# Kernel optimization log

Hardware: AMD Instinct MI355X
Metric: run time of the kernel (lower is better)

## Reference

```python
import jax, jax.numpy as jnp
import numpy as np

E = 512        # emb_size
H = 2 * E      # LSTM units
B = 512        # beam/query batch (batched Python-loop states)
K = 32         # padded candidates per state
T = 8          # max_path_length
N_ENT = 50000
N_REL = 5000


def setup_inputs() -> dict:
    key = jax.random.key(0)
    ks = jax.random.split(key, 12)
    f32 = jnp.float32
    ent_emb = jax.random.normal(ks[0], (N_ENT, E), f32) * 0.05
    rel_emb = jax.random.normal(ks[1], (N_REL, E), f32) * 0.05
    relation = jax.random.normal(ks[2], (B, E), f32) * 0.05
    Wx = jax.random.normal(ks[3], (H, 4 * H), f32) * 0.02
    Wh = jax.random.normal(ks[4], (H, 4 * H), f32) * 0.02
    b = jnp.zeros((4 * H,), f32)
    W1 = jax.random.normal(ks[5], (4 * E, 3 * E), f32) * 0.02
    b1 = jnp.zeros((3 * E,), f32)
    W2 = jax.random.normal(ks[6], (3 * E, 2 * E), f32) * 0.02
    b2 = jnp.zeros((2 * E,), f32)
    current_ids = jax.random.randint(ks[7], (T, B), 0, N_ENT)
    prev_rel_ids = jax.random.randint(ks[8], (T, B), 0, N_REL)
    cand_rel_ids = jax.random.randint(ks[9], (T, B, K), 0, N_REL)
    cand_ent_ids = jax.random.randint(ks[10], (T, B, K), 0, N_ENT)
    return {
        "ent_emb": ent_emb, "rel_emb": rel_emb, "relation": relation,
        "Wx": Wx, "Wh": Wh, "b": b,
        "W1": W1, "b1": b1, "W2": W2, "b2": b2,
        "current_ids": current_ids, "prev_rel_ids": prev_rel_ids,
        "cand_rel_ids": cand_rel_ids, "cand_ent_ids": cand_ent_ids,
    }


def reference(ent_emb, rel_emb, relation, Wx, Wh, b, W1, b1, W2, b2,
              current_ids, prev_rel_ids, cand_rel_ids, cand_ent_ids):
    Bh = relation.shape[0]
    units = Wh.shape[0]
    h0 = jnp.zeros((Bh, units), ent_emb.dtype)
    c0 = jnp.zeros((Bh, units), ent_emb.dtype)

    def step(carry, xs):
        h, c = carry
        cur, prl, crel, cent = xs
        # LSTMCell input: concat(prev relation vec, current entity vec)  [B, 2E]
        x = jnp.concatenate([rel_emb[prl], ent_emb[cur]], axis=-1)
        z = x @ Wx + h @ Wh + b                      # [B, 4H], keras gate order i,f,g,o
        i_, f_, g_, o_ = jnp.split(z, 4, axis=-1)
        c = jax.nn.sigmoid(f_) * c + jax.nn.sigmoid(i_) * jnp.tanh(g_)
        h = jax.nn.sigmoid(o_) * jnp.tanh(c)
        # posterior MLP on concat(ent, history, relation)  [B, 4E] -> [B, 2E]
        feat = jax.nn.relu(jnp.concatenate([ent_emb[cur], h, relation], axis=-1) @ W1 + b1)
        feat = jax.nn.relu(feat @ W2 + b2)
        # candidate embeddings: concat(rel vec, to-entity vec)  [B, K, 2E]
        cand = jnp.concatenate([rel_emb[crel], ent_emb[cent]], axis=-1)
        probs = jax.nn.softmax(jnp.einsum('bkd,bd->bk', cand, feat), axis=-1)
        return (h, c), probs

    _, probs = jax.lax.scan(step, (h0, c0),
                            (current_ids, prev_rel_ids, cand_rel_ids, cand_ent_ids))
    return probs  # [T, B, K]
```

## Files before the change

kernel.cpp:

```cpp
#include <hip/hip_runtime.h>
#include <stdint.h>

typedef __attribute__((ext_vector_type(4))) float f32x4;
typedef __attribute__((ext_vector_type(8))) __bf16 bf16x8;
typedef __attribute__((ext_vector_type(8))) unsigned short u16x8;
typedef __attribute__((ext_vector_type(4))) unsigned short u16x4;

__device__ __forceinline__ float b2f(unsigned short u) {
  unsigned int x = ((unsigned int)u) << 16;
  float f; __builtin_memcpy(&f, &x, 4); return f;
}
__device__ __forceinline__ unsigned short f2b(float f) {
  unsigned int x; __builtin_memcpy(&x, &f, 4);
  x += 0x7fffu + ((x >> 16) & 1u);
  return (unsigned short)(x >> 16);
}
__device__ __forceinline__ float sigmoidf(float x) {
  return 1.f / (1.f + __expf(-x));
}
__device__ __forceinline__ float tanh_fast(float x) {
  return 1.f - 2.f / (1.f + __expf(2.f * x));
}

__global__ __launch_bounds__(256) void transpose_f2b(
    const float* __restrict__ in, unsigned short* __restrict__ out,
    int R, int C) {
  __shared__ unsigned short tile[64][72];
  const int r0 = blockIdx.y * 64, c0 = blockIdx.x * 64;
  const int tid = threadIdx.x;
  const int r = tid >> 3;
  const int c8 = (tid & 7) * 8;
#pragma unroll
  for (int i = 0; i < 2; i++) {
    const float* src = in + (size_t)(r0 + r + 32*i) * C + c0 + c8;
    f32x4 a = *(const f32x4*)src;
    f32x4 b = *(const f32x4*)(src + 4);
    unsigned short tmp[8];
#pragma unroll
    for (int j = 0; j < 4; j++) { tmp[j] = f2b(a[j]); tmp[4+j] = f2b(b[j]); }
    *(u16x8*)(&tile[r + 32*i][c8]) = *(u16x8*)tmp;
  }
  __syncthreads();
#pragma unroll
  for (int i = 0; i < 2; i++) {
    const int ro = r + 32*i;
    unsigned short tmp[8];
#pragma unroll
    for (int j = 0; j < 8; j++) tmp[j] = tile[c8 + j][ro];
    *(u16x8*)(out + (size_t)(c0 + ro) * R + r0 + c8) = *(u16x8*)tmp;
  }
}

__global__ void gather_all(const float* __restrict__ ent,
                           const float* __restrict__ rel,
                           const float* __restrict__ relation,
                           const int* __restrict__ cur, const int* __restrict__ prl,
                           unsigned short* __restrict__ Xall,
                           unsigned short* __restrict__ ERall) {
  const int row = blockIdx.x;
  const int b = row & 511;
  const int tid = threadIdx.x;
  const int ci = cur[row], ri = prl[row];
  const float* xsrc = (tid < 64) ? (rel + (size_t)ri * 512 + tid * 8)
                                 : (ent + (size_t)ci * 512 + (tid - 64) * 8);
  const float* esrc = (tid < 64) ? (ent + (size_t)ci * 512 + tid * 8)
                                 : (relation + (size_t)b * 512 + (tid - 64) * 8);
  f32x4 xa = *(const f32x4*)xsrc, xb = *(const f32x4*)(xsrc + 4);
  f32x4 ea = *(const f32x4*)esrc, eb = *(const f32x4*)(esrc + 4);
  unsigned short xt[8], et[8];
#pragma unroll
  for (int j = 0; j < 4; j++) {
    xt[j] = f2b(xa[j]); xt[4+j] = f2b(xb[j]);
    et[j] = f2b(ea[j]); et[4+j] = f2b(eb[j]);
  }
  *(u16x8*)(Xall + (size_t)row * 1024 + tid * 8) = *(u16x8*)xt;
  *(u16x8*)(ERall + (size_t)row * 1024 + tid * 8) = *(u16x8*)et;
}

template<bool HAS_PRE, bool HAS_BIAS, bool DO_RELU, bool PERM_B>
__global__ __launch_bounds__(256) void gemm_bf16(
    const unsigned short* __restrict__ A, int lda,
    const unsigned short* __restrict__ BT, int ldb,
    int K, int ksplit, int koff0, int koff1,
    const unsigned short* __restrict__ pre, int ldpre,
    const float* __restrict__ bias,
    unsigned short* __restrict__ Cout, int ldc) {
  __shared__ unsigned short As[128][72];
  __shared__ unsigned short Bs[128][72];
  const int tid = threadIdx.x;
  const int lane = tid & 63;
  const int w = tid >> 6;
  const int wr = w >> 1, wc = w & 1;
  const int m0 = blockIdx.y * 128, n0 = blockIdx.x * 128;
  f32x4 acc[4][4] = {};
  const int rs = tid >> 3;
  const int cs = (tid & 7) * 8;

  for (int k0 = 0; k0 < K; k0 += 64) {
    const int keff = (k0 < ksplit) ? (k0 + koff0) : (k0 + koff1);
#pragma unroll
    for (int i = 0; i < 4; i++)
      *(u16x8*)(&As[rs + 32*i][cs]) =
          *(const u16x8*)(A + (size_t)(m0 + rs + 32*i) * lda + k0 + cs);
#pragma unroll
    for (int i = 0; i < 4; i++) {
      const int brow = n0 + rs + 32*i;
      const int prow = PERM_B ? (((brow & 3) << 10) + (brow >> 2)) : brow;
      *(u16x8*)(&Bs[rs + 32*i][cs]) =
          *(const u16x8*)(BT + (size_t)prow * ldb + keff + cs);
    }
    __syncthreads();
#pragma unroll
    for (int ks = 0; ks < 2; ks++) {
      const int kb = ks * 32 + (lane >> 4) * 8;
      bf16x8 af[4], bfr[4];
#pragma unroll
      for (int m = 0; m < 4; m++)
        af[m] = *reinterpret_cast<const bf16x8*>(&As[wr*64 + m*16 + (lane & 15)][kb]);
#pragma unroll
      for (int n = 0; n < 4; n++)
        bfr[n] = *reinterpret_cast<const bf16x8*>(&Bs[wc*64 + n*16 + (lane & 15)][kb]);
#pragma unroll
      for (int m = 0; m < 4; m++)
#pragma unroll
        for (int n = 0; n < 4; n++)
          acc[m][n] = __builtin_amdgcn_mfma_f32_16x16x32_bf16(af[m], bfr[n], acc[m][n], 0, 0, 0);
    }
    __syncthreads();
  }

  const int cn = lane & 15, rb = (lane >> 4) * 4;
#pragma unroll
  for (int m = 0; m < 4; m++) {
#pragma unroll
    for (int n = 0; n < 4; n++) {
      const int gn = n0 + wc*64 + n*16 + cn;
#pragma unroll
      for (int r = 0; r < 4; r++) {
        const int gm = m0 + wr*64 + m*16 + rb + r;
        float v = acc[m][n][r];
        if (HAS_PRE)  v += b2f(pre[(size_t)gm * ldpre + gn]);
        if (HAS_BIAS) v += bias[gn];
        if (DO_RELU)  v = v > 0.f ? v : 0.f;
        Cout[(size_t)gm * ldc + gn] = f2b(v);
      }
    }
  }
}

__global__ __launch_bounds__(512) void zgemm_lstm(
    const unsigned short* __restrict__ A,
    const unsigned short* __restrict__ BT,
    const unsigned short* __restrict__ pre,
    const float* __restrict__ bias,
    unsigned short* __restrict__ Hout,
    float* __restrict__ Cst) {
  __shared__ unsigned short As[2][64][72];
  __shared__ unsigned short Bs[2][128][72];
  __shared__ f32x4 accL[8][256];
  const int tid = threadIdx.x;
  const int lane = tid & 63;
  const int w = tid >> 6;
  const int q = w >> 2;
  const int wq = w & 3;
  const int wr = wq >> 1, wc = wq & 1;
  const int m0 = blockIdx.y * 64, n0 = blockIdx.x * 128;
  f32x4 acc[2][4] = {};
  const int tq = tid & 255;
  const int rs = tq >> 3;
  const int cs = (tq & 7) * 8;

  for (int k0 = 0; k0 < 512; k0 += 64) {
    const int kk = q * 512 + k0;
#pragma unroll
    for (int i = 0; i < 2; i++)
      *(u16x8*)(&As[q][rs + 32*i][cs]) =
          *(const u16x8*)(A + (size_t)(m0 + rs + 32*i) * 1024 + kk + cs);
#pragma unroll
    for (int i = 0; i < 4; i++) {
      const int brow = n0 + rs + 32*i;
      const int prow = ((brow & 3) << 10) + (brow >> 2);
      *(u16x8*)(&Bs[q][rs + 32*i][cs]) =
          *(const u16x8*)(BT + (size_t)prow * 1024 + kk + cs);
    }
    __syncthreads();
#pragma unroll
    for (int ks = 0; ks < 2; ks++) {
      const int kb = ks * 32 + (lane >> 4) * 8;
      bf16x8 af[2], bfr[4];
#pragma unroll
      for (int m = 0; m < 2; m++)
        af[m] = *reinterpret_cast<const bf16x8*>(&As[q][wr*32 + m*16 + (lane & 15)][kb]);
#pragma unroll
      for (int n = 0; n < 4; n++)
        bfr[n] = *reinterpret_cast<const bf16x8*>(&Bs[q][wc*64 + n*16 + (lane & 15)][kb]);
#pragma unroll
      for (int m = 0; m < 2; m++)
#pragma unroll
        for (int n = 0; n < 4; n++)
          acc[m][n] = __builtin_amdgcn_mfma_f32_16x16x32_bf16(af[m], bfr[n], acc[m][n], 0, 0, 0);
    }
    __syncthreads();
  }

  if (q == 1) {
#pragma unroll
    for (int m = 0; m < 2; m++)
#pragma unroll
      for (int n = 0; n < 4; n++)
        accL[m*4 + n][tq] = acc[m][n];
  }
  __syncthreads();
  if (q == 0) {
    const int cn = lane & 15, rb = (lane >> 4) * 4, g = lane & 3;
#pragma unroll
    for (int m = 0; m < 2; m++) {
#pragma unroll
      for (int n = 0; n < 4; n++) {
        const f32x4 s4 = accL[m*4 + n][tq];
        const int gn = n0 + wc*64 + n*16 + cn;
        const int u = gn >> 2;
        const float gb = bias[g * 1024 + u];
        const int row0 = m0 + wr*32 + m*16 + rb;
        const float v0 = acc[m][n][0] + s4[0] + b2f(pre[(size_t)(row0+0) * 4096 + gn]) + gb;
        const float v1 = acc[m][n][1] + s4[1] + b2f(pre[(size_t)(row0+1) * 4096 + gn]) + gb;
        const float v2 = acc[m][n][2] + s4[2] + b2f(pre[(size_t)(row0+2) * 4096 + gn]) + gb;
        const float v3 = acc[m][n][3] + s4[3] + b2f(pre[(size_t)(row0+3) * 4096 + gn]) + gb;
        auto sel = [&](int idx) {
          return idx == 0 ? v0 : idx == 1 ? v1 : idx == 2 ? v2 : v3;
        };
        const float own = sel(g);
        const float r1 = __shfl_xor(sel(g ^ 1), 1);
        const float r2 = __shfl_xor(sel(g ^ 2), 2);
        const float r3 = __shfl_xor(sel(g ^ 3), 3);
        const float zi = g==0 ? own : g==1 ? r1 : g==2 ? r2 : r3;
        const float zf = g==0 ? r1  : g==1 ? own: g==2 ? r3 : r2;
        const float zg_= g==0 ? r2  : g==1 ? r3 : g==2 ? own: r1;
        const float zo = g==0 ? r3  : g==1 ? r2 : g==2 ? r1 : own;
        const size_t hidx = (size_t)(row0 + g) * 1024 + u;
        const float cnew = sigmoidf(zf) * Cst[hidx] + sigmoidf(zi) * tanh_fast(zg_);
        const float h = sigmoidf(zo) * tanh_fast(cnew);
        Cst[hidx] = cnew;
        Hout[hidx] = f2b(h);
      }
    }
  }
}

__global__ void lstm_gate0(const unsigned short* __restrict__ P1_,
                           const float* __restrict__ bias,
                           float* __restrict__ C, unsigned short* __restrict__ H) {
  const int idx = blockIdx.x * 256 + threadIdx.x;
  const int b = idx >> 10, u = idx & 1023;
  u16x4 z4 = *(const u16x4*)(P1_ + (size_t)b * 4096 + 4 * u);
  const float i_ = b2f(z4[0]) + bias[u];
  const float g_ = b2f(z4[2]) + bias[2048 + u];
  const float o_ = b2f(z4[3]) + bias[3072 + u];
  const float c = sigmoidf(i_) * tanh_fast(g_);
  const float h = sigmoidf(o_) * tanh_fast(c);
  C[idx] = c;
  H[idx] = f2b(h);
}

__global__ __launch_bounds__(256) void score_softmax(
    const unsigned short* __restrict__ F2,
    const float* __restrict__ rel,
    const float* __restrict__ ent,
    const int* __restrict__ crel, const int* __restrict__ cent,
    float* __restrict__ outp) {
  const int b = blockIdx.x;
  const int tid = threadIdx.x;
  const int lane = tid & 63, w = tid >> 6;
  __shared__ float feat[1024];
  __shared__ float logits[32];
  {
    u16x4 fv = ((const u16x4*)(F2 + (size_t)b * 1024))[tid];
#pragma unroll
    for (int j = 0; j < 4; j++) feat[tid * 4 + j] = b2f(fv[j]);
  }
  __syncthreads();
  for (int k = w; k < 32; k += 4) {
    const int ri = crel[b * 32 + k], ei = cent[b * 32 + k];
    const float* rp = rel + (size_t)ri * 512 + lane * 8;
    const float* ep = ent + (size_t)ei * 512 + lane * 8;
    f32x4 r0 = *(const f32x4*)rp, r1 = *(const f32x4*)(rp + 4);
    f32x4 e0 = *(const f32x4*)ep, e1 = *(const f32x4*)(ep + 4);
    float sum = 0.f;
#pragma unroll
    for (int j = 0; j < 4; j++) {
      sum += r0[j] * feat[lane * 8 + j];
      sum += r1[j] * feat[lane * 8 + 4 + j];
      sum += e0[j] * feat[512 + lane * 8 + j];
      sum += e1[j] * feat[512 + lane * 8 + 4 + j];
    }
#pragma unroll
    for (int off = 32; off; off >>= 1) sum += __shfl_down(sum, off, 64);
    if (lane == 0) logits[k] = sum;
  }
  __syncthreads();
  if (tid < 32) {
    const float l = logits[tid];
    float mx = l;
#pragma unroll
    for (int off = 16; off; off >>= 1) mx = fmaxf(mx, __shfl_xor(mx, off, 32));
    const float p = __expf(l - mx);
    float s = p;
#pragma unroll
    for (int off = 16; off; off >>= 1) s += __shfl_xor(s, off, 32);
    outp[(size_t)b * 32 + tid] = p / s;
  }
}

extern "C" void kernel_launch(void* const* d_in, const int* in_sizes, int n_in,
                              void* d_out, int out_size, void* d_ws, size_t ws_size,
                              hipStream_t stream) {
  const float* ent      = (const float*)d_in[0];
  const float* rel      = (const float*)d_in[1];
  const float* relation = (const float*)d_in[2];
  const float* Wx       = (const float*)d_in[3];
  const float* Wh       = (const float*)d_in[4];
  const float* bvec     = (const float*)d_in[5];
  const float* W1       = (const float*)d_in[6];
  const float* b1       = (const float*)d_in[7];
  const float* W2       = (const float*)d_in[8];
  const float* b2       = (const float*)d_in[9];
  const int* cur  = (const int*)d_in[10];
  const int* prl  = (const int*)d_in[11];
  const int* crel = (const int*)d_in[12];
  const int* cent = (const int*)d_in[13];
  float* out = (float*)d_out;
  (void)in_sizes; (void)n_in; (void)out_size; (void)ws_size;

  char* wsp = (char*)d_ws;
  auto alloc = [&](size_t bytes) { char* p = wsp; wsp += (bytes + 255) & ~(size_t)255; return p; };
  unsigned short* WxT  = (unsigned short*)alloc((size_t)4096 * 1024 * 2);
  unsigned short* WhT  = (unsigned short*)alloc((size_t)4096 * 1024 * 2);
  unsigned short* W1T  = (unsigned short*)alloc((size_t)1536 * 2048 * 2);
  unsigned short* W2T  = (unsigned short*)alloc((size_t)1024 * 1536 * 2);
  unsigned short* Xall = (unsigned short*)alloc((size_t)4096 * 1024 * 2);
  unsigned short* ERall= (unsigned short*)alloc((size_t)4096 * 1024 * 2);
  unsigned short* P1   = (unsigned short*)alloc((size_t)4096 * 4096 * 2);
  unsigned short* P2   = (unsigned short*)alloc((size_t)4096 * 1536 * 2);
  unsigned short* Hall = (unsigned short*)alloc((size_t)4096 * 1024 * 2);
  unsigned short* F1   = (unsigned short*)alloc((size_t)4096 * 1536 * 2);
  unsigned short* F2   = (unsigned short*)alloc((size_t)4096 * 1024 * 2);
  float*          C    = (float*)         alloc((size_t)512 * 1024 * 4);

  const dim3 blk(256);
  const int BIG = 1 << 30;
  const size_t HS = (size_t)512 * 1024;

  transpose_f2b<<<dim3(4096/64, 1024/64), blk, 0, stream>>>(Wx, WxT, 1024, 4096);
  transpose_f2b<<<dim3(4096/64, 1024/64), blk, 0, stream>>>(Wh, WhT, 1024, 4096);
  transpose_f2b<<<dim3(1536/64, 2048/64), blk, 0, stream>>>(W1, W1T, 2048, 1536);
  transpose_f2b<<<dim3(1024/64, 1536/64), blk, 0, stream>>>(W2, W2T, 1536, 1024);
  gather_all<<<4096, 128, 0, stream>>>(ent, rel, relation, cur, prl, Xall, ERall);

  gemm_bf16<false,false,false,true><<<dim3(32, 32), blk, 0, stream>>>(
      Xall, 1024, WxT, 1024, 1024, BIG, 0, 0, nullptr, 0, nullptr, P1, 4096);
  gemm_bf16<false,false,false,false><<<dim3(12, 32), blk, 0, stream>>>(
      ERall, 1024, W1T, 2048, 1024, 512, 0, 1024, nullptr, 0, nullptr, P2, 1536);

  lstm_gate0<<<2048, 256, 0, stream>>>(P1, bvec, C, Hall);
  for (int t = 1; t < 8; t++) {
    zgemm_lstm<<<dim3(32, 8), dim3(512), 0, stream>>>(
        Hall + (size_t)(t - 1) * HS, WhT,
        P1 + (size_t)t * 512 * 4096, bvec,
        Hall + (size_t)t * HS, C);
  }

  gemm_bf16<true,true,true,false><<<dim3(12, 32), blk, 0, stream>>>(
      Hall, 1024, W1T, 2048, 1024, BIG, 512, 0, P2, 1536, b1, F1, 1536);
  gemm_bf16<false,true,true,false><<<dim3(8, 32), blk, 0, stream>>>(
      F1, 1536, W2T, 1536, 1536, BIG, 0, 0, nullptr, 0, b2, F2, 1024);
  score_softmax<<<4096, 256, 0, stream>>>(F2, rel, ent, crel, cent, out);
}
```

Before: 358.4 us.

## Pre-convert embedding tables to bf16 and merge the split W1 GEMM

```diff
diff --git a/kernel.cpp b/kernel.cpp
--- a/kernel.cpp
+++ b/kernel.cpp
@@ -20,6 +20,17 @@
 }
 __device__ __forceinline__ float tanh_fast(float x) {
   return 1.f - 2.f / (1.f + __expf(2.f * x));
+}
+
+__global__ __launch_bounds__(256) void conv_f2b(
+    const float* __restrict__ in, unsigned short* __restrict__ out) {
+  const int i = blockIdx.x * 256 + threadIdx.x;
+  f32x4 a = *(const f32x4*)(in + (size_t)i * 8);
+  f32x4 b = *(const f32x4*)(in + (size_t)i * 8 + 4);
+  unsigned short t[8];
+#pragma unroll
+  for (int j = 0; j < 4; j++) { t[j] = f2b(a[j]); t[4+j] = f2b(b[j]); }
+  *(u16x8*)(out + (size_t)i * 8) = *(u16x8*)t;
 }
 
 __global__ __launch_bounds__(256) void transpose_f2b(
@@ -51,9 +62,9 @@
   }
 }
 
-__global__ void gather_all(const float* __restrict__ ent,
-                           const float* __restrict__ rel,
-                           const float* __restrict__ relation,
+__global__ void gather_all(const unsigned short* __restrict__ entB,
+                           const unsigned short* __restrict__ relB,
+                           const unsigned short* __restrict__ relationB,
                            const int* __restrict__ cur, const int* __restrict__ prl,
                            unsigned short* __restrict__ Xall,
                            unsigned short* __restrict__ ERall) {
@@ -61,28 +72,19 @@
   const int b = row & 511;
   const int tid = threadIdx.x;
   const int ci = cur[row], ri = prl[row];
-  const float* xsrc = (tid < 64) ? (rel + (size_t)ri * 512 + tid * 8)
-                                 : (ent + (size_t)ci * 512 + (tid - 64) * 8);
-  const float* esrc = (tid < 64) ? (ent + (size_t)ci * 512 + tid * 8)
-                                 : (relation + (size_t)b * 512 + (tid - 64) * 8);
-  f32x4 xa = *(const f32x4*)xsrc, xb = *(const f32x4*)(xsrc + 4);
-  f32x4 ea = *(const f32x4*)esrc, eb = *(const f32x4*)(esrc + 4);
-  unsigned short xt[8], et[8];
-#pragma unroll
-  for (int j = 0; j < 4; j++) {
-    xt[j] = f2b(xa[j]); xt[4+j] = f2b(xb[j]);
-    et[j] = f2b(ea[j]); et[4+j] = f2b(eb[j]);
-  }
-  *(u16x8*)(Xall + (size_t)row * 1024 + tid * 8) = *(u16x8*)xt;
-  *(u16x8*)(ERall + (size_t)row * 1024 + tid * 8) = *(u16x8*)et;
-}
-
-template<bool HAS_PRE, bool HAS_BIAS, bool DO_RELU, bool PERM_B>
+  const unsigned short* xsrc = (tid < 64) ? (relB + (size_t)ri * 512 + tid * 8)
+                                          : (entB + (size_t)ci * 512 + (tid - 64) * 8);
+  const unsigned short* esrc = (tid < 64) ? (entB + (size_t)ci * 512 + tid * 8)
+                                          : (relationB + (size_t)b * 512 + (tid - 64) * 8);
+  *(u16x8*)(Xall + (size_t)row * 1024 + tid * 8) = *(const u16x8*)xsrc;
+  *(u16x8*)(ERall + (size_t)row * 1024 + tid * 8) = *(const u16x8*)esrc;
+}
+
+template<bool HAS_BIAS, bool DO_RELU, bool PERM_B, bool ASPLIT>
 __global__ __launch_bounds__(256) void gemm_bf16(
-    const unsigned short* __restrict__ A, int lda,
-    const unsigned short* __restrict__ BT, int ldb,
-    int K, int ksplit, int koff0, int koff1,
-    const unsigned short* __restrict__ pre, int ldpre,
+    const unsigned short* __restrict__ A,
+    const unsigned short* __restrict__ A2, int lda,
+    const unsigned short* __restrict__ BT, int ldb, int K,
     const float* __restrict__ bias,
     unsigned short* __restrict__ Cout, int ldc) {
   __shared__ unsigned short As[128][72];
@@ -97,17 +99,22 @@
   const int cs = (tid & 7) * 8;
 
   for (int k0 = 0; k0 < K; k0 += 64) {
-    const int keff = (k0 < ksplit) ? (k0 + koff0) : (k0 + koff1);
+    const unsigned short* asrc; int ac;
+    if (ASPLIT) {
+      if (k0 < 512)       { asrc = A;  ac = k0; }
+      else if (k0 < 1536) { asrc = A2; ac = k0 - 512; }
+      else                { asrc = A;  ac = k0 - 1024; }
+    } else { asrc = A; ac = k0; }
 #pragma unroll
     for (int i = 0; i < 4; i++)
       *(u16x8*)(&As[rs + 32*i][cs]) =
-          *(const u16x8*)(A + (size_t)(m0 + rs + 32*i) * lda + k0 + cs);
+          *(const u16x8*)(asrc + (size_t)(m0 + rs + 32*i) * lda + ac + cs);
 #pragma unroll
     for (int i = 0; i < 4; i++) {
       const int brow = n0 + rs + 32*i;
       const int prow = PERM_B ? (((brow & 3) << 10) + (brow >> 2)) : brow;
       *(u16x8*)(&Bs[rs + 32*i][cs]) =
-          *(const u16x8*)(BT + (size_t)prow * ldb + keff + cs);
+          *(const u16x8*)(BT + (size_t)prow * ldb + k0 + cs);
     }
     __syncthreads();
 #pragma unroll
@@ -139,7 +146,6 @@
       for (int r = 0; r < 4; r++) {
         const int gm = m0 + wr*64 + m*16 + rb + r;
         float v = acc[m][n][r];
-        if (HAS_PRE)  v += b2f(pre[(size_t)gm * ldpre + gn]);
         if (HAS_BIAS) v += bias[gn];
         if (DO_RELU)  v = v > 0.f ? v : 0.f;
         Cout[(size_t)gm * ldc + gn] = f2b(v);
@@ -264,8 +270,8 @@
 
 __global__ __launch_bounds__(256) void score_softmax(
     const unsigned short* __restrict__ F2,
-    const float* __restrict__ rel,
-    const float* __restrict__ ent,
+    const unsigned short* __restrict__ relB,
+    const unsigned short* __restrict__ entB,
     const int* __restrict__ crel, const int* __restrict__ cent,
     float* __restrict__ outp) {
   const int b = blockIdx.x;
@@ -281,17 +287,13 @@
   __syncthreads();
   for (int k = w; k < 32; k += 4) {
     const int ri = crel[b * 32 + k], ei = cent[b * 32 + k];
-    const float* rp = rel + (size_t)ri * 512 + lane * 8;
-    const float* ep = ent + (size_t)ei * 512 + lane * 8;
-    f32x4 r0 = *(const f32x4*)rp, r1 = *(const f32x4*)(rp + 4);
-    f32x4 e0 = *(const f32x4*)ep, e1 = *(const f32x4*)(ep + 4);
+    u16x8 rv = *(const u16x8*)(relB + (size_t)ri * 512 + lane * 8);
+    u16x8 ev = *(const u16x8*)(entB + (size_t)ei * 512 + lane * 8);
     float sum = 0.f;
 #pragma unroll
-    for (int j = 0; j < 4; j++) {
-      sum += r0[j] * feat[lane * 8 + j];
-      sum += r1[j] * feat[lane * 8 + 4 + j];
-      sum += e0[j] * feat[512 + lane * 8 + j];
-      sum += e1[j] * feat[512 + lane * 8 + 4 + j];
+    for (int j = 0; j < 8; j++) {
+      sum += b2f(rv[j]) * feat[lane * 8 + j];
+      sum += b2f(ev[j]) * feat[512 + lane * 8 + j];
     }
 #pragma unroll
     for (int off = 32; off; off >>= 1) sum += __shfl_down(sum, off, 64);
@@ -333,6 +335,9 @@
 
   char* wsp = (char*)d_ws;
   auto alloc = [&](size_t bytes) { char* p = wsp; wsp += (bytes + 255) & ~(size_t)255; return p; };
+  unsigned short* entB = (unsigned short*)alloc((size_t)50000 * 512 * 2);
+  unsigned short* relB = (unsigned short*)alloc((size_t)5000 * 512 * 2);
+  unsigned short* rlnB = (unsigned short*)alloc((size_t)512 * 512 * 2);
   unsigned short* WxT  = (unsigned short*)alloc((size_t)4096 * 1024 * 2);
   unsigned short* WhT  = (unsigned short*)alloc((size_t)4096 * 1024 * 2);
   unsigned short* W1T  = (unsigned short*)alloc((size_t)1536 * 2048 * 2);
@@ -340,26 +345,25 @@
   unsigned short* Xall = (unsigned short*)alloc((size_t)4096 * 1024 * 2);
   unsigned short* ERall= (unsigned short*)alloc((size_t)4096 * 1024 * 2);
   unsigned short* P1   = (unsigned short*)alloc((size_t)4096 * 4096 * 2);
-  unsigned short* P2   = (unsigned short*)alloc((size_t)4096 * 1536 * 2);
   unsigned short* Hall = (unsigned short*)alloc((size_t)4096 * 1024 * 2);
   unsigned short* F1   = (unsigned short*)alloc((size_t)4096 * 1536 * 2);
   unsigned short* F2   = (unsigned short*)alloc((size_t)4096 * 1024 * 2);
   float*          C    = (float*)         alloc((size_t)512 * 1024 * 4);
 
   const dim3 blk(256);
-  const int BIG = 1 << 30;
   const size_t HS = (size_t)512 * 1024;
 
+  conv_f2b<<<50000 * 512 / 8 / 256, blk, 0, stream>>>(ent, entB);
+  conv_f2b<<<5000 * 512 / 8 / 256, blk, 0, stream>>>(rel, relB);
+  conv_f2b<<<512 * 512 / 8 / 256, blk, 0, stream>>>(relation, rlnB);
   transpose_f2b<<<dim3(4096/64, 1024/64), blk, 0, stream>>>(Wx, WxT, 1024, 4096);
   transpose_f2b<<<dim3(4096/64, 1024/64), blk, 0, stream>>>(Wh, WhT, 1024, 4096);
   transpose_f2b<<<dim3(1536/64, 2048/64), blk, 0, stream>>>(W1, W1T, 2048, 1536);
   transpose_f2b<<<dim3(1024/64, 1536/64), blk, 0, stream>>>(W2, W2T, 1536, 1024);
-  gather_all<<<4096, 128, 0, stream>>>(ent, rel, relation, cur, prl, Xall, ERall);
-
-  gemm_bf16<false,false,false,true><<<dim3(32, 32), blk, 0, stream>>>(
-      Xall, 1024, WxT, 1024, 1024, BIG, 0, 0, nullptr, 0, nullptr, P1, 4096);
-  gemm_bf16<false,false,false,false><<<dim3(12, 32), blk, 0, stream>>>(
-      ERall, 1024, W1T, 2048, 1024, 512, 0, 1024, nullptr, 0, nullptr, P2, 1536);
+  gather_all<<<4096, 128, 0, stream>>>(entB, relB, rlnB, cur, prl, Xall, ERall);
+
+  gemm_bf16<false,false,true,false><<<dim3(32, 32), blk, 0, stream>>>(
+      Xall, nullptr, 1024, WxT, 1024, 1024, nullptr, P1, 4096);
 
   lstm_gate0<<<2048, 256, 0, stream>>>(P1, bvec, C, Hall);
   for (int t = 1; t < 8; t++) {
@@ -369,9 +373,9 @@
         Hall + (size_t)t * HS, C);
   }
 
-  gemm_bf16<true,true,true,false><<<dim3(12, 32), blk, 0, stream>>>(
-      Hall, 1024, W1T, 2048, 1024, BIG, 512, 0, P2, 1536, b1, F1, 1536);
-  gemm_bf16<false,true,true,false><<<dim3(8, 32), blk, 0, stream>>>(
-      F1, 1536, W2T, 1536, 1536, BIG, 0, 0, nullptr, 0, b2, F2, 1024);
-  score_softmax<<<4096, 256, 0, stream>>>(F2, rel, ent, crel, cent, out);
-}
+  gemm_bf16<true,true,false,true><<<dim3(12, 32), blk, 0, stream>>>(
+      ERall, Hall, 1024, W1T, 2048, 2048, b1, F1, 1536);
+  gemm_bf16<true,true,false,false><<<dim3(8, 32), blk, 0, stream>>>(
+      F1, nullptr, 1536, W2T, 1536, 1536, b2, F2, 1024);
+  score_softmax<<<4096, 256, 0, stream>>>(F2, relB, entB, crel, cent, out);
+}
```

New measurement: 348.2 us. -2.8%, faster.
